# Performance work log

Hardware: AMD Instinct MI355X
Metric: run time of the kernel (lower is better)

The kernel has to match this reference:

```python
import jax, jax.numpy as jnp
import numpy as np

BATCH = 16384
N_FEATURES = 768
FT_OUT = 1024
ACTIVE_P = 32.0 / 768.0  # ~32 active features per board, like real positions


def setup_inputs() -> dict:
    key = jax.random.key(0)
    k1, k2, k3, k4, k5, k6 = jax.random.split(key, 6)
    # densified sparse one-hot boards: binary {0,1} with ~32/768 density
    board_stm = (jax.random.uniform(k1, (BATCH, N_FEATURES)) < ACTIVE_P).astype(jnp.float32)
    board_nstm = (jax.random.uniform(k2, (BATCH, N_FEATURES)) < ACTIVE_P).astype(jnp.float32)
    # Linear(768, FT_OUT): weight [out, in], bias [out]
    W_ft = jax.random.normal(k3, (FT_OUT, N_FEATURES), dtype=jnp.float32) * (1.0 / np.sqrt(N_FEATURES))
    b_ft = jax.random.normal(k4, (FT_OUT,), dtype=jnp.float32) * 0.01
    # Linear(2*FT_OUT, 1)
    W_out = jax.random.normal(k5, (1, 2 * FT_OUT), dtype=jnp.float32) * (1.0 / np.sqrt(2 * FT_OUT))
    b_out = jax.random.normal(k6, (1,), dtype=jnp.float32) * 0.01
    return {"board_stm": board_stm, "board_nstm": board_nstm,
            "W_ft": W_ft, "b_ft": b_ft, "W_out": W_out, "b_out": b_out}


def screlu(x):
    # SCReLU: clamp(x, 0, 1)^2
    return jnp.square(jnp.clip(x, 0.0, 1.0))


def reference(board_stm, board_nstm, W_ft, b_ft, W_out, b_out):
    # feature transformer applied to both perspectives (shared weights)
    stm = jnp.einsum('bf,of->bo', board_stm, W_ft) + b_ft   # [B, FT_OUT]
    nstm = jnp.einsum('bf,of->bo', board_nstm, W_ft) + b_ft  # [B, FT_OUT]
    hidden = screlu(jnp.concatenate([stm, nstm], axis=1))    # [B, 2*FT_OUT]
    out = jnp.einsum('bh,oh->bo', hidden, W_out) + b_out     # [B, 1]
    return jax.nn.sigmoid(out)
```

## Files before the change

### kernel.cpp

```cpp
#include <hip/hip_runtime.h>
#include <stdint.h>

#define BATCH 16384
#define NF 768
#define FT 1024
#define DUMMY NF
#define PAD_M 4

__global__ __launch_bounds__(192) void prep_wq(const float* __restrict__ W_ft,
                                               unsigned char* __restrict__ Wq,
                                               float* __restrict__ invs) {
    const int o = blockIdx.x;
    const int t = threadIdx.x;
    __shared__ float smax[3];
    __shared__ float sscale;
    const float4 v = *(const float4*)(W_ft + (size_t)o * NF + t * 4);
    float m = fmaxf(fmaxf(fabsf(v.x), fabsf(v.y)), fmaxf(fabsf(v.z), fabsf(v.w)));
    #pragma unroll
    for (int s = 32; s > 0; s >>= 1) m = fmaxf(m, __shfl_down(m, s, 64));
    if ((t & 63) == 0) smax[t >> 6] = m;
    __syncthreads();
    if (t == 0) {
        const float am = fmaxf(fmaxf(smax[0], smax[1]), smax[2]);
        sscale = 127.0f / am;
        invs[o] = am / 127.0f;
        Wq[(size_t)DUMMY * FT + o] = 128;
    }
    __syncthreads();
    const float s = sscale;
    const float arr[4] = {v.x, v.y, v.z, v.w};
    #pragma unroll
    for (int j = 0; j < 4; ++j) {
        const int q = (int)rintf(arr[j] * s);
        Wq[(size_t)(t * 4 + j) * FT + o] = (unsigned char)(q + 128);
    }
}

__global__ __launch_bounds__(256) void nnue_fwd(
    const float* __restrict__ bstm, const float* __restrict__ bnstm,
    const unsigned char* __restrict__ Wq, const float* __restrict__ invs,
    const float* __restrict__ b_ft, const float* __restrict__ W_out,
    const float* __restrict__ b_out, float* __restrict__ out)
{
    const int t = threadIdx.x;
    const int wv = t >> 6;
    const int lane = t & 63;
    const int row = blockIdx.x * 2 + (wv >> 1);
    const int p = wv & 1;

    __shared__ int fidx[4][NF + PAD_M];
    __shared__ float red[4];

    const float* board = (p ? bnstm : bstm) + (size_t)row * NF;
    int base = 0;
    #pragma unroll
    for (int c = 0; c < 3; ++c) {
        const float4 v = *(const float4*)(board + lane * 12 + c * 4);
        const float arr[4] = {v.x, v.y, v.z, v.w};
        #pragma unroll
        for (int j = 0; j < 4; ++j) {
            const bool nz = (arr[j] != 0.0f);
            const uint64_t m = __ballot(nz);
            if (nz) {
                const int pos = base + __popcll(m & ((1ull << lane) - 1ull));
                fidx[wv][pos] = lane * 12 + c * 4 + j;
            }
            base += __popcll(m);
        }
    }
    const int padded = (base + PAD_M - 1) & ~(PAD_M - 1);
    if (lane < padded - base) fidx[wv][base + lane] = DUMMY;

    uint32_t accE[4] = {0, 0, 0, 0}, accO[4] = {0, 0, 0, 0};
    const unsigned char* wbase = Wq + lane * 16;
    for (int i0 = 0; i0 < padded; i0 += 4) {
        const int4 fi = *(const int4*)&fidx[wv][i0];
        const int f0 = __builtin_amdgcn_readfirstlane(fi.x);
        const int f1 = __builtin_amdgcn_readfirstlane(fi.y);
        const int f2 = __builtin_amdgcn_readfirstlane(fi.z);
        const int f3 = __builtin_amdgcn_readfirstlane(fi.w);
        const uint4 w0 = *(const uint4*)(wbase + (size_t)f0 * FT);
        const uint4 w1 = *(const uint4*)(wbase + (size_t)f1 * FT);
        const uint4 w2 = *(const uint4*)(wbase + (size_t)f2 * FT);
        const uint4 w3 = *(const uint4*)(wbase + (size_t)f3 * FT);
        const uint32_t wc[4][4] = {{w0.x, w0.y, w0.z, w0.w},
                                   {w1.x, w1.y, w1.z, w1.w},
                                   {w2.x, w2.y, w2.z, w2.w},
                                   {w3.x, w3.y, w3.z, w3.w}};
        #pragma unroll
        for (int r = 0; r < 4; ++r)
            #pragma unroll
            for (int k = 0; k < 4; ++k) {
                accE[k] += wc[r][k] & 0x00FF00FFu;
                accO[k] += (wc[r][k] >> 8) & 0x00FF00FFu;
            }
    }

    const int obase = lane * 16;
    const float fcorr = 128.0f * (float)padded;
    float partial = 0.0f;
    #pragma unroll
    for (int k = 0; k < 4; ++k) {
        const int o0 = obase + 4 * k;
        const float4 iv = *(const float4*)(invs + o0);
        const float4 bv = *(const float4*)(b_ft + o0);
        const float4 wo = *(const float4*)(W_out + p * FT + o0);
        const float sums[4] = {(float)(int)(accE[k] & 0xFFFFu),
                               (float)(int)(accO[k] & 0xFFFFu),
                               (float)(int)(accE[k] >> 16),
                               (float)(int)(accO[k] >> 16)};
        const float ivv[4] = {iv.x, iv.y, iv.z, iv.w};
        const float bvv[4] = {bv.x, bv.y, bv.z, bv.w};
        const float wov[4] = {wo.x, wo.y, wo.z, wo.w};
        #pragma unroll
        for (int j = 0; j < 4; ++j) {
            float h = fmaf(sums[j] - fcorr, ivv[j], bvv[j]);
            h = fminf(fmaxf(h, 0.0f), 1.0f);
            partial = fmaf(h * h, wov[j], partial);
        }
    }

    #pragma unroll
    for (int s = 32; s > 0; s >>= 1) partial += __shfl_down(partial, s, 64);
    if (lane == 0) red[wv] = partial;
    __syncthreads();
    if ((t & 127) == 0) {
        const int r = wv >> 1;
        const float x = red[2 * r] + red[2 * r + 1] + b_out[0];
        out[blockIdx.x * 2 + r] = 1.0f / (1.0f + expf(-x));
    }
}

extern "C" void kernel_launch(void* const* d_in, const int* in_sizes, int n_in,
                              void* d_out, int out_size, void* d_ws, size_t ws_size,
                              hipStream_t stream) {
    const float* board_stm  = (const float*)d_in[0];
    const float* board_nstm = (const float*)d_in[1];
    const float* W_ft       = (const float*)d_in[2];
    const float* b_ft       = (const float*)d_in[3];
    const float* W_out      = (const float*)d_in[4];
    const float* b_out      = (const float*)d_in[5];
    float* out = (float*)d_out;

    unsigned char* Wq = (unsigned char*)d_ws;
    float* invs = (float*)((char*)d_ws + (size_t)(NF + 1) * FT);

    prep_wq<<<FT, 192, 0, stream>>>(W_ft, Wq, invs);
    nnue_fwd<<<BATCH / 2, 256, 0, stream>>>(board_stm, board_nstm, Wq, invs,
                                            b_ft, W_out, b_out, out);
}
```

Measured before the change: 80.33 us.

## Replace sparse gather-accumulate with dense int8 MFMA over packed boards

Replaces the per-row sparse index gather and byte-packed SIMD accumulation with a dense int8 GEMM on matrix cores. Each block converts 32 rows of both boards to int8 0/1 in LDS, and each wave computes 128 output columns using mfma_i32_16x16x64_i8 against row-major signed int8 weights. The SCReLU and output dot product run on the accumulators. This does all 768 features instead of about 32 active ones, but each block now reads the whole quantized weight matrix once for 64 rows instead of issuing scattered per-row loads.

Result: faster. 76.21 us (-5.1%).

```diff
diff --git a/kernel.cpp b/kernel.cpp
--- a/kernel.cpp
+++ b/kernel.cpp
@@ -4,11 +4,16 @@
 #define BATCH 16384
 #define NF 768
 #define FT 1024
-#define DUMMY NF
-#define PAD_M 4
+#define RB 32
+#define GR (2 * RB)
+#define ALD 784
+#define NW 8
+#define THREADS 512
+
+typedef int i32x4 __attribute__((ext_vector_type(4)));
 
 __global__ __launch_bounds__(192) void prep_wq(const float* __restrict__ W_ft,
-                                               unsigned char* __restrict__ Wq,
+                                               char* __restrict__ Wq,
                                                float* __restrict__ invs) {
     const int o = blockIdx.x;
     const int t = threadIdx.x;
@@ -24,110 +29,111 @@
         const float am = fmaxf(fmaxf(smax[0], smax[1]), smax[2]);
         sscale = 127.0f / am;
         invs[o] = am / 127.0f;
-        Wq[(size_t)DUMMY * FT + o] = 128;
     }
     __syncthreads();
     const float s = sscale;
     const float arr[4] = {v.x, v.y, v.z, v.w};
+    uint32_t pk = 0;
     #pragma unroll
     for (int j = 0; j < 4; ++j) {
         const int q = (int)rintf(arr[j] * s);
-        Wq[(size_t)(t * 4 + j) * FT + o] = (unsigned char)(q + 128);
+        pk |= ((uint32_t)(unsigned char)(char)q) << (8 * j);
     }
+    *(uint32_t*)(Wq + (size_t)o * NF + t * 4) = pk;
 }
 
-__global__ __launch_bounds__(256) void nnue_fwd(
+__global__ __launch_bounds__(THREADS, 2) void nnue_mfma(
     const float* __restrict__ bstm, const float* __restrict__ bnstm,
-    const unsigned char* __restrict__ Wq, const float* __restrict__ invs,
+    const char* __restrict__ Wq, const float* __restrict__ invs,
     const float* __restrict__ b_ft, const float* __restrict__ W_out,
     const float* __restrict__ b_out, float* __restrict__ out)
 {
+    __shared__ __align__(16) char Albs[GR * ALD];
+    __shared__ float red[GR][NW];
+
     const int t = threadIdx.x;
-    const int wv = t >> 6;
-    const int lane = t & 63;
-    const int row = blockIdx.x * 2 + (wv >> 1);
-    const int p = wv & 1;
+    const int w = t >> 6;
+    const int l = t & 63;
+    const int b0 = blockIdx.x * RB;
 
-    __shared__ int fidx[4][NF + PAD_M];
-    __shared__ float red[4];
+    #pragma unroll
+    for (int it = 0; it < 24; ++it) {
+        const int g = it * THREADS + t;
+        const int row = g / 192;
+        const int c4 = g - row * 192;
+        const float* src = (row < RB) ? (bstm + (size_t)(b0 + row) * NF)
+                                      : (bnstm + (size_t)(b0 + row - RB) * NF);
+        const float4 v = *(const float4*)(src + c4 * 4);
+        const uint32_t pk = (uint32_t)(v.x != 0.0f)
+                          | ((uint32_t)(v.y != 0.0f) << 8)
+                          | ((uint32_t)(v.z != 0.0f) << 16)
+                          | ((uint32_t)(v.w != 0.0f) << 24);
+        *(uint32_t*)(Albs + row * ALD + c4 * 4) = pk;
+    }
+    __syncthreads();
 
-    const float* board = (p ? bnstm : bstm) + (size_t)row * NF;
-    int base = 0;
-    #pragma unroll
-    for (int c = 0; c < 3; ++c) {
-        const float4 v = *(const float4*)(board + lane * 12 + c * 4);
-        const float arr[4] = {v.x, v.y, v.z, v.w};
+    i32x4 acc[4][8] = {};
+    const int cl = l & 15;
+    const int q = l >> 4;
+    const char* bptr = Wq + (size_t)(w * 128 + cl) * NF + q * 16;
+    const int aoff = cl * ALD + q * 16;
+
+    #pragma unroll 2
+    for (int ks = 0; ks < 12; ++ks) {
+        i32x4 bfrag[8];
         #pragma unroll
-        for (int j = 0; j < 4; ++j) {
-            const bool nz = (arr[j] != 0.0f);
-            const uint64_t m = __ballot(nz);
-            if (nz) {
-                const int pos = base + __popcll(m & ((1ull << lane) - 1ull));
-                fidx[wv][pos] = lane * 12 + c * 4 + j;
-            }
-            base += __popcll(m);
-        }
-    }
-    const int padded = (base + PAD_M - 1) & ~(PAD_M - 1);
-    if (lane < padded - base) fidx[wv][base + lane] = DUMMY;
-
-    uint32_t accE[4] = {0, 0, 0, 0}, accO[4] = {0, 0, 0, 0};
-    const unsigned char* wbase = Wq + lane * 16;
-    for (int i0 = 0; i0 < padded; i0 += 4) {
-        const int4 fi = *(const int4*)&fidx[wv][i0];
-        const int f0 = __builtin_amdgcn_readfirstlane(fi.x);
-        const int f1 = __builtin_amdgcn_readfirstlane(fi.y);
-        const int f2 = __builtin_amdgcn_readfirstlane(fi.z);
-        const int f3 = __builtin_amdgcn_readfirstlane(fi.w);
-        const uint4 w0 = *(const uint4*)(wbase + (size_t)f0 * FT);
-        const uint4 w1 = *(const uint4*)(wbase + (size_t)f1 * FT);
-        const uint4 w2 = *(const uint4*)(wbase + (size_t)f2 * FT);
-        const uint4 w3 = *(const uint4*)(wbase + (size_t)f3 * FT);
-        const uint32_t wc[4][4] = {{w0.x, w0.y, w0.z, w0.w},
-                                   {w1.x, w1.y, w1.z, w1.w},
-                                   {w2.x, w2.y, w2.z, w2.w},
-                                   {w3.x, w3.y, w3.z, w3.w}};
+        for (int c = 0; c < 8; ++c)
+            bfrag[c] = *(const i32x4*)(bptr + c * 16 * NF + ks * 64);
+        i32x4 afrag[4];
+        #pragma unroll
+        for (int r = 0; r < 4; ++r)
+            afrag[r] = *(const i32x4*)(Albs + aoff + r * 16 * ALD + ks * 64);
         #pragma unroll
         for (int r = 0; r < 4; ++r)
             #pragma unroll
-            for (int k = 0; k < 4; ++k) {
-                accE[k] += wc[r][k] & 0x00FF00FFu;
-                accO[k] += (wc[r][k] >> 8) & 0x00FF00FFu;
-            }
+            for (int c = 0; c < 8; ++c)
+                acc[r][c] = __builtin_amdgcn_mfma_i32_16x16x64_i8(
+                    afrag[r], bfrag[c], acc[r][c], 0, 0, 0);
     }
 
-    const int obase = lane * 16;
-    const float fcorr = 128.0f * (float)padded;
-    float partial = 0.0f;
+    float ps[4][4] = {};
     #pragma unroll
-    for (int k = 0; k < 4; ++k) {
-        const int o0 = obase + 4 * k;
-        const float4 iv = *(const float4*)(invs + o0);
-        const float4 bv = *(const float4*)(b_ft + o0);
-        const float4 wo = *(const float4*)(W_out + p * FT + o0);
-        const float sums[4] = {(float)(int)(accE[k] & 0xFFFFu),
-                               (float)(int)(accO[k] & 0xFFFFu),
-                               (float)(int)(accE[k] >> 16),
-                               (float)(int)(accO[k] >> 16)};
-        const float ivv[4] = {iv.x, iv.y, iv.z, iv.w};
-        const float bvv[4] = {bv.x, bv.y, bv.z, bv.w};
-        const float wov[4] = {wo.x, wo.y, wo.z, wo.w};
+    for (int c = 0; c < 8; ++c) {
+        const int col = w * 128 + c * 16 + cl;
+        const float iv = invs[col];
+        const float bf = b_ft[col];
+        const float wo0 = W_out[col];
+        const float wo1 = W_out[FT + col];
+        #pragma unroll
+        for (int r = 0; r < 4; ++r) {
+            const float wo = (r < 2) ? wo0 : wo1;
+            #pragma unroll
+            for (int j = 0; j < 4; ++j) {
+                float h = fmaf((float)acc[r][c][j], iv, bf);
+                h = fminf(fmaxf(h, 0.0f), 1.0f);
+                ps[r][j] = fmaf(h * h, wo, ps[r][j]);
+            }
+        }
+    }
+    #pragma unroll
+    for (int r = 0; r < 4; ++r)
         #pragma unroll
         for (int j = 0; j < 4; ++j) {
-            float h = fmaf(sums[j] - fcorr, ivv[j], bvv[j]);
-            h = fminf(fmaxf(h, 0.0f), 1.0f);
-            partial = fmaf(h * h, wov[j], partial);
+            float v = ps[r][j];
+            v += __shfl_xor(v, 1, 64);
+            v += __shfl_xor(v, 2, 64);
+            v += __shfl_xor(v, 4, 64);
+            v += __shfl_xor(v, 8, 64);
+            if (cl == 0) red[16 * r + 4 * q + j][w] = v;
         }
-    }
+    __syncthreads();
 
-    #pragma unroll
-    for (int s = 32; s > 0; s >>= 1) partial += __shfl_down(partial, s, 64);
-    if (lane == 0) red[wv] = partial;
-    __syncthreads();
-    if ((t & 127) == 0) {
-        const int r = wv >> 1;
-        const float x = red[2 * r] + red[2 * r + 1] + b_out[0];
-        out[blockIdx.x * 2 + r] = 1.0f / (1.0f + expf(-x));
+    if (t < RB) {
+        float x = b_out[0];
+        #pragma unroll
+        for (int w2 = 0; w2 < NW; ++w2)
+            x += red[t][w2] + red[RB + t][w2];
+        out[b0 + t] = 1.0f / (1.0f + expf(-x));
     }
 }
 
@@ -142,10 +148,10 @@
     const float* b_out      = (const float*)d_in[5];
     float* out = (float*)d_out;
 
-    unsigned char* Wq = (unsigned char*)d_ws;
-    float* invs = (float*)((char*)d_ws + (size_t)(NF + 1) * FT);
+    char* Wq = (char*)d_ws;
+    float* invs = (float*)((char*)d_ws + (size_t)FT * NF);
 
     prep_wq<<<FT, 192, 0, stream>>>(W_ft, Wq, invs);
-    nnue_fwd<<<BATCH / 2, 256, 0, stream>>>(board_stm, board_nstm, Wq, invs,
-                                            b_ft, W_out, b_out, out);
+    nnue_mfma<<<BATCH / RB, THREADS, 0, stream>>>(board_stm, board_nstm, Wq, invs,
+                                                  b_ft, W_out, b_out, out);
 }
```
